# Performance work log

Hardware: AMD Instinct MI355X
Metric: run time of the kernel (lower is better)

## Reference

```python
import jax, jax.numpy as jnp
import numpy as np

N_AGENTS = 8
N_ACTIONS = 16
SAMPLE = 16
STATE_DIM = 256
EMBED = 256
IN_DIM = N_AGENTS * N_ACTIONS + STATE_DIM  # 384


def setup_inputs() -> dict:
    key = jax.random.key(0)
    ks = jax.random.split(key, 12)
    bs, t = 32, 32
    s = 0.05
    return {
        "states": jax.random.normal(ks[0], (bs, t, STATE_DIM), jnp.float32),
        "agent_qs": jax.random.normal(ks[1], (bs, t, N_AGENTS, N_ACTIONS), jnp.float32),
        "W1": jax.random.normal(ks[2], (IN_DIM, EMBED), jnp.float32) * s,
        "b1": jnp.zeros((EMBED,), jnp.float32),
        "W2": jax.random.normal(ks[3], (EMBED, EMBED), jnp.float32) * s,
        "b2": jnp.zeros((EMBED,), jnp.float32),
        "W3": jax.random.normal(ks[4], (EMBED, 1), jnp.float32) * s,
        "b3": jnp.zeros((1,), jnp.float32),
        "Vw1": jax.random.normal(ks[5], (STATE_DIM, EMBED), jnp.float32) * s,
        "Vb1": jnp.zeros((EMBED,), jnp.float32),
        "Vw2": jax.random.normal(ks[6], (EMBED, 1), jnp.float32) * s,
        "Vb2": jnp.zeros((1,), jnp.float32),
    }


def reference(states, agent_qs, W1, b1, W2, b2, W3, b3, Vw1, Vb1, Vw2, Vb2):
    bs, t = states.shape[0], states.shape[1]
    B = bs * t
    A, NA, S, sd = N_AGENTS, N_ACTIONS, SAMPLE, STATE_DIM
    st = states.reshape(B, sd)
    qs = agent_qs.reshape(B, A, NA)

    # --- sample grand coalitions (random permutation per (B,S) row) ---
    perm_key = jax.random.key(42)
    u = jax.random.uniform(perm_key, (B, S, A))
    pos = jnp.argsort(u, axis=-1)          # grand_coalitions_pos: agent i -> position pos[i]
    inv = jnp.argsort(pos, axis=-1)        # grand_coalitions: position j -> agent inv[j]

    indiv = jax.nn.one_hot(pos, A, dtype=st.dtype)                         # (B,S,A,A)
    subcoal = (jnp.arange(A)[None, None, None, :] <= pos[..., None]).astype(st.dtype)
    no_i = subcoal - indiv                                                 # coalition members excl. self

    # reorder agent qs along position dim: reordered[b,s,j,:] = qs[b, inv[b,s,j], :]
    reordered = jnp.take_along_axis(
        jnp.broadcast_to(qs[:, None], (B, S, A, NA)), inv[..., None], axis=2)

    # (B,S,A,A,NA): detach contribution of other coalition members
    coal = (jax.lax.stop_gradient(reordered[:, :, None] * no_i[..., None])
            + reordered[:, :, None] * indiv[..., None])

    x = coal.reshape(B * S * A, A * NA)
    stx = jnp.broadcast_to(st[:, None, None], (B, S, A, sd)).reshape(B * S * A, sd)
    inp = jnp.concatenate([stx, x], axis=1)

    h = jax.nn.relu(inp @ W1 + b1)
    h = jax.nn.relu(h @ W2 + b2)
    advs = h @ W3 + b3
    v = jax.nn.relu(stx @ Vw1 + Vb1) @ Vw2 + Vb2

    marginal = (advs + v).reshape(B, S, A)
    shapley = marginal.mean(axis=1)        # mean over samples
    return shapley.reshape(bs, t, A)
```

## Files before the change

kernel.cpp:

```cpp
#include <hip/hip_runtime.h>


#define A_N   8
#define NA_N  16
#define S_N   16
#define SD    256
#define EMB   256
#define B_TOT 1024

typedef __bf16 bf16x8 __attribute__((ext_vector_type(8)));
typedef float  f32x4  __attribute__((ext_vector_type(4)));

__device__ __forceinline__ f32x4 splat4(float v) {
  f32x4 x; x[0] = v; x[1] = v; x[2] = v; x[3] = v; return x;
}
__device__ __forceinline__ bf16x8 zero8() {
  bf16x8 z;
#pragma unroll
  for (int j = 0; j < 8; ++j) z[j] = (__bf16)0.0f;
  return z;
}

__device__ __forceinline__ float jax_uniform(unsigned idx) {
  const unsigned ks0 = 0u, ks1 = 42u, ks2 = 0x1BD11BDAu ^ 42u;
  unsigned x0 = 0u + ks0;
  unsigned x1 = idx + ks1;
#define TF_RND(r) { x0 += x1; x1 = (x1 << (r)) | (x1 >> (32 - (r))); x1 ^= x0; }
  TF_RND(13) TF_RND(15) TF_RND(26) TF_RND(6)  x0 += ks1; x1 += ks2 + 1u;
  TF_RND(17) TF_RND(29) TF_RND(16) TF_RND(24) x0 += ks2; x1 += ks0 + 2u;
  TF_RND(13) TF_RND(15) TF_RND(26) TF_RND(6)  x0 += ks0; x1 += ks1 + 3u;
  TF_RND(17) TF_RND(29) TF_RND(16) TF_RND(24) x0 += ks1; x1 += ks2 + 4u;
  TF_RND(13) TF_RND(15) TF_RND(26) TF_RND(6)  x0 += ks2; x1 += ks0 + 5u;
#undef TF_RND
  const unsigned bits = x0 ^ x1;
  return __uint_as_float((bits >> 9) | 0x3F800000u) - 1.0f;
}

__global__ __launch_bounds__(256) void prep_kernel(
    const float* __restrict__ states, const float* __restrict__ W1,
    const float* __restrict__ b1, const float* __restrict__ Vw1,
    const float* __restrict__ Vb1, const float* __restrict__ Vw2,
    const float* __restrict__ Vb2, float* __restrict__ sW,
    float* __restrict__ vout) {
  __shared__ float st_l[2][SD];
  __shared__ float red_l[2][4];
  const int b0 = blockIdx.x * 2;
  const int n = threadIdx.x;

#pragma unroll
  for (int i = 0; i < 2; ++i) st_l[i][n] = states[(b0 + i) * SD + n];
  __syncthreads();

  float aS[2], aV[2];
  const float b1n = b1[n], vb1n = Vb1[n];
#pragma unroll
  for (int i = 0; i < 2; ++i) { aS[i] = b1n; aV[i] = vb1n; }

#pragma unroll 8
  for (int k = 0; k < SD; ++k) {
    const float wv = W1[k * EMB + n];
    const float vw = Vw1[k * EMB + n];
#pragma unroll
    for (int i = 0; i < 2; ++i) {
      const float s = st_l[i][k];
      aS[i] = fmaf(s, wv, aS[i]);
      aV[i] = fmaf(s, vw, aV[i]);
    }
  }
#pragma unroll
  for (int i = 0; i < 2; ++i) sW[(b0 + i) * EMB + n] = aS[i];

  const float vw2 = Vw2[n];
#pragma unroll
  for (int i = 0; i < 2; ++i) {
    float c = fmaxf(aV[i], 0.f) * vw2;
#pragma unroll
    for (int off = 32; off; off >>= 1) c += __shfl_down(c, off);
    if ((n & 63) == 0) red_l[i][n >> 6] = c;
  }
  __syncthreads();
  if (n < 2)
    vout[b0 + n] = red_l[n][0] + red_l[n][1] + red_l[n][2] + red_l[n][3] + Vb2[0];
}

__global__ __launch_bounds__(256) void pack_kernel(
    const float* __restrict__ W1, const float* __restrict__ W2,
    __bf16* __restrict__ W1b_bf, __bf16* __restrict__ W2_bf) {
  const int ts = blockIdx.x * 256 + threadIdx.x;
  if (ts < 4096) {
    const int t = ts >> 10, rem = ts & 1023, u = rem >> 6, L = rem & 63;
    const int q = L >> 4, l15 = L & 15;
#pragma unroll
    for (int j = 0; j < 8; ++j) {
      const int k = t * 32 + q * 8 + j, nn = u * 16 + l15;
      W1b_bf[ts * 8 + j] = (__bf16)W1[(SD + k) * EMB + nn];
    }
  } else {
    const int ts2 = ts - 4096;
    const int t = ts2 >> 10, rem = ts2 & 1023, u = rem >> 6, L = rem & 63;
    const int q = L >> 4, l15 = L & 15;
#pragma unroll
    for (int j = 0; j < 8; ++j) {
      const int k = t * 32 + q * 8 + j, nn = u * 16 + l15;
      W2_bf[ts2 * 8 + j] = (__bf16)W2[k * EMB + nn];
    }
  }
}

__global__ __launch_bounds__(256, 4) void main_kernel(
    const float* __restrict__ agent_qs, const float* __restrict__ b2g,
    const float* __restrict__ W3, const float* __restrict__ b3,
    const float* __restrict__ sW, const float* __restrict__ vv,
    const __bf16* __restrict__ W1b_bf, const __bf16* __restrict__ W2_bf,
    float* __restrict__ out) {
  __shared__ bf16x8 h1_l[32 * 64];
  __shared__ __attribute__((aligned(16))) __bf16 qs_bf[A_N * NA_N];
  __shared__ float u_l[128];
  __shared__ int   inv_l[128];
  __shared__ int   pos_l[128];
  __shared__ float adv_part[4][64];
  __shared__ float marg_l[128];

  const int b = blockIdx.x;
  const int n = threadIdx.x;
  const int w = n >> 6, L = n & 63, q = L >> 4, l15 = L & 15;

  if (n < 128) {
    qs_bf[n] = (__bf16)agent_qs[b * 128 + n];
    u_l[n] = jax_uniform((unsigned)(b * 128 + n));
  }
  __syncthreads();

  if (n < 128) {
    const int s = n >> 3, a = n & 7;
    const float u = u_l[n];
    int r = 0;
#pragma unroll
    for (int a2 = 0; a2 < A_N; ++a2) {
      const float u2 = u_l[s * 8 + a2];
      r += (u2 < u || (u2 == u && a2 < a)) ? 1 : 0;
    }
    inv_l[n] = r;
    pos_l[s * 8 + r] = a;
  }
  __syncthreads();

  const int i_pref  = l15 & 7;
  const int sl_half = l15 >> 3;
  const int jq      = q >> 1;
  const int na0     = (q & 1) * 8;

  for (int p = 0; p < 2; ++p) {
#pragma unroll 1
    for (int nh = 0; nh < 2; ++nh) {
      f32x4 acc[4][2];
#pragma unroll
      for (int i = 0; i < 2; ++i) {
        const float sv = sW[b * EMB + (w * 4 + nh * 2 + i) * 16 + l15];
#pragma unroll
        for (int mt = 0; mt < 4; ++mt) acc[mt][i] = splat4(sv);
      }
#pragma unroll 2
      for (int t = 0; t < 4; ++t) {
        const int jcoal = t * 2 + jq;
        const bool on = (jcoal <= i_pref);
        bf16x8 bfr[2];
#pragma unroll
        for (int i = 0; i < 2; ++i)
          bfr[i] = *(const bf16x8*)
              &W1b_bf[((t * 16 + w * 4 + nh * 2 + i) * 64 + L) * 8];
#pragma unroll
        for (int mt = 0; mt < 4; ++mt) {
          const int ag = inv_l[(p * 8 + mt * 2 + sl_half) * 8 + jcoal];
          const bf16x8 qv = *(const bf16x8*)&qs_bf[ag * NA_N + na0];
          const bf16x8 af = on ? qv : zero8();
#pragma unroll
          for (int i = 0; i < 2; ++i)
            acc[mt][i] = __builtin_amdgcn_mfma_f32_16x16x32_bf16(
                af, bfr[i], acc[mt][i], 0, 0, 0);
        }
      }
      __bf16* h1e = (__bf16*)h1_l;
#pragma unroll
      for (int i = 0; i < 2; ++i) {
        const int c = (w * 4 + nh * 2 + i) * 16 + l15;
        const int t2 = c >> 5, q2 = (c >> 3) & 3, j2 = l15 & 7;
#pragma unroll
        for (int mt = 0; mt < 4; ++mt) {
#pragma unroll
          for (int r = 0; r < 4; ++r) {
            const float v = fmaxf(acc[mt][i][r], 0.f);
            h1e[(((t2 * 4 + mt) * 64) + q2 * 16 + q * 4 + r) * 8 + j2] =
                (__bf16)v;
          }
        }
      }
    }
    __syncthreads();

    float psum[4][4];
#pragma unroll
    for (int mt = 0; mt < 4; ++mt)
#pragma unroll
      for (int r = 0; r < 4; ++r) psum[mt][r] = 0.f;

#pragma unroll 1
    for (int nh = 0; nh < 2; ++nh) {
      f32x4 acc[4][2];
#pragma unroll
      for (int i = 0; i < 2; ++i) {
        const float bv = b2g[(w * 4 + nh * 2 + i) * 16 + l15];
#pragma unroll
        for (int mt = 0; mt < 4; ++mt) acc[mt][i] = splat4(bv);
      }
#pragma unroll 2
      for (int t = 0; t < 8; ++t) {
        bf16x8 bfr[2];
#pragma unroll
        for (int i = 0; i < 2; ++i)
          bfr[i] = *(const bf16x8*)
              &W2_bf[((t * 16 + w * 4 + nh * 2 + i) * 64 + L) * 8];
#pragma unroll
        for (int mt = 0; mt < 4; ++mt) {
          const bf16x8 af = h1_l[(t * 4 + mt) * 64 + L];
#pragma unroll
          for (int i = 0; i < 2; ++i)
            acc[mt][i] = __builtin_amdgcn_mfma_f32_16x16x32_bf16(
                af, bfr[i], acc[mt][i], 0, 0, 0);
        }
      }
#pragma unroll
      for (int i = 0; i < 2; ++i) {
        const float w3v = W3[(w * 4 + nh * 2 + i) * 16 + l15];
#pragma unroll
        for (int mt = 0; mt < 4; ++mt)
#pragma unroll
          for (int r = 0; r < 4; ++r)
            psum[mt][r] = fmaf(fmaxf(acc[mt][i][r], 0.f), w3v, psum[mt][r]);
      }
    }

#pragma unroll
    for (int mt = 0; mt < 4; ++mt) {
#pragma unroll
      for (int r = 0; r < 4; ++r) {
        float sum = psum[mt][r];
#pragma unroll
        for (int off = 1; off < 16; off <<= 1) sum += __shfl_xor(sum, off);
        if (l15 == 0) adv_part[w][mt * 16 + q * 4 + r] = sum;
      }
    }
    __syncthreads();
    if (n < 64)
      marg_l[p * 64 + n] = adv_part[0][n] + adv_part[1][n] +
                           adv_part[2][n] + adv_part[3][n];
    __syncthreads();
  }

  if (n < A_N) {
    float sh = 0.f;
#pragma unroll
    for (int s = 0; s < S_N; ++s) sh += marg_l[s * 8 + pos_l[s * 8 + n]];
    out[b * A_N + n] = sh * (1.f / 16.f) + b3[0] + vv[b];
  }
}

extern "C" void kernel_launch(void* const* d_in, const int* in_sizes, int n_in,
                              void* d_out, int out_size, void* d_ws,
                              size_t ws_size, hipStream_t stream) {
  const float* states   = (const float*)d_in[0];
  const float* agent_qs = (const float*)d_in[1];
  const float* W1       = (const float*)d_in[2];
  const float* b1       = (const float*)d_in[3];
  const float* W2       = (const float*)d_in[4];
  const float* b2       = (const float*)d_in[5];
  const float* W3       = (const float*)d_in[6];
  const float* b3       = (const float*)d_in[7];
  const float* Vw1      = (const float*)d_in[8];
  const float* Vb1      = (const float*)d_in[9];
  const float* Vw2      = (const float*)d_in[10];
  const float* Vb2      = (const float*)d_in[11];
  float* out = (float*)d_out;

  char* ws = (char*)d_ws;
  float*  sW     = (float*)(ws);
  float*  vv     = (float*)(ws + 1048576);
  __bf16* W1b_bf = (__bf16*)(ws + 1052672);
  __bf16* W2_bf  = (__bf16*)(ws + 1118208);

  prep_kernel<<<512, 256, 0, stream>>>(states, W1, b1, Vw1, Vb1, Vw2, Vb2,
                                       sW, vv);
  pack_kernel<<<48, 256, 0, stream>>>(W1, W2, W1b_bf, W2_bf);
  main_kernel<<<B_TOT, 256, 0, stream>>>(agent_qs, b2, W3, b3, sW, vv,
                                         W1b_bf, W2_bf, out);
}
```

Before: 123.0 us.

## Merge prep/pack kernels, skip zero coalition MFMAs, widen tiles, swizzle LDS

Folds the weight-packing kernel into the prep kernel to drop one launch. Reorders the main kernel's first-layer M tiles so each tile maps to one coalition position, which lets it skip the MFMAs whose inputs are entirely masked to zero. Both GEMM stages now handle four N columns per wave in one pass instead of two half passes, with biases and W3 preloaded into registers. The h1 shared-memory layout gets an XOR swizzle to avoid bank conflicts, and the final gather is remapped to match. Raising register use may cut occupancy, so launch bounds drop from 4 to 3 blocks.

```diff
diff --git a/kernel.cpp b/kernel.cpp
--- a/kernel.cpp
+++ b/kernel.cpp
@@ -36,14 +36,39 @@
   return __uint_as_float((bits >> 9) | 0x3F800000u) - 1.0f;
 }
 
-__global__ __launch_bounds__(256) void prep_kernel(
+__global__ __launch_bounds__(256) void prep_pack_kernel(
     const float* __restrict__ states, const float* __restrict__ W1,
     const float* __restrict__ b1, const float* __restrict__ Vw1,
     const float* __restrict__ Vb1, const float* __restrict__ Vw2,
-    const float* __restrict__ Vb2, float* __restrict__ sW,
-    float* __restrict__ vout) {
+    const float* __restrict__ Vb2, const float* __restrict__ W2,
+    float* __restrict__ sW, float* __restrict__ vout,
+    __bf16* __restrict__ W1b_bf, __bf16* __restrict__ W2_bf) {
   __shared__ float st_l[2][SD];
   __shared__ float red_l[2][4];
+
+  if (blockIdx.x >= 512) {
+    const int ts = (blockIdx.x - 512) * 256 + threadIdx.x;
+    if (ts < 4096) {
+      const int t = ts >> 10, rem = ts & 1023, u = rem >> 6, Lp = rem & 63;
+      const int qp = Lp >> 4, l15p = Lp & 15;
+#pragma unroll
+      for (int j = 0; j < 8; ++j) {
+        const int k = t * 32 + qp * 8 + j, nn = u * 16 + l15p;
+        W1b_bf[ts * 8 + j] = (__bf16)W1[(SD + k) * EMB + nn];
+      }
+    } else {
+      const int ts2 = ts - 4096;
+      const int t = ts2 >> 10, rem = ts2 & 1023, u = rem >> 6, Lp = rem & 63;
+      const int qp = Lp >> 4, l15p = Lp & 15;
+#pragma unroll
+      for (int j = 0; j < 8; ++j) {
+        const int k = t * 32 + qp * 8 + j, nn = u * 16 + l15p;
+        W2_bf[ts2 * 8 + j] = (__bf16)W2[k * EMB + nn];
+      }
+    }
+    return;
+  }
+
   const int b0 = blockIdx.x * 2;
   const int n = threadIdx.x;
 
@@ -83,31 +108,7 @@
     vout[b0 + n] = red_l[n][0] + red_l[n][1] + red_l[n][2] + red_l[n][3] + Vb2[0];
 }
 
-__global__ __launch_bounds__(256) void pack_kernel(
-    const float* __restrict__ W1, const float* __restrict__ W2,
-    __bf16* __restrict__ W1b_bf, __bf16* __restrict__ W2_bf) {
-  const int ts = blockIdx.x * 256 + threadIdx.x;
-  if (ts < 4096) {
-    const int t = ts >> 10, rem = ts & 1023, u = rem >> 6, L = rem & 63;
-    const int q = L >> 4, l15 = L & 15;
-#pragma unroll
-    for (int j = 0; j < 8; ++j) {
-      const int k = t * 32 + q * 8 + j, nn = u * 16 + l15;
-      W1b_bf[ts * 8 + j] = (__bf16)W1[(SD + k) * EMB + nn];
-    }
-  } else {
-    const int ts2 = ts - 4096;
-    const int t = ts2 >> 10, rem = ts2 & 1023, u = rem >> 6, L = rem & 63;
-    const int q = L >> 4, l15 = L & 15;
-#pragma unroll
-    for (int j = 0; j < 8; ++j) {
-      const int k = t * 32 + q * 8 + j, nn = u * 16 + l15;
-      W2_bf[ts2 * 8 + j] = (__bf16)W2[k * EMB + nn];
-    }
-  }
-}
-
-__global__ __launch_bounds__(256, 4) void main_kernel(
+__global__ __launch_bounds__(256, 3) void main_kernel(
     const float* __restrict__ agent_qs, const float* __restrict__ b2g,
     const float* __restrict__ W3, const float* __restrict__ b3,
     const float* __restrict__ sW, const float* __restrict__ vv,
@@ -124,6 +125,11 @@
   const int b = blockIdx.x;
   const int n = threadIdx.x;
   const int w = n >> 6, L = n & 63, q = L >> 4, l15 = L & 15;
+  const int s7 = l15 & 7;
+  const int sl = l15 >> 3;
+  const int jq = q >> 1;
+  const int na0 = (q & 1) * 8;
+  const int Lsw = L ^ ((L >> 3) & 3);
 
   if (n < 128) {
     qs_bf[n] = (__bf16)agent_qs[b * 128 + n];
@@ -145,100 +151,99 @@
   }
   __syncthreads();
 
-  const int i_pref  = l15 & 7;
-  const int sl_half = l15 >> 3;
-  const int jq      = q >> 1;
-  const int na0     = (q & 1) * 8;
-
+  const bool diag_on = (jq <= sl);
+
+  float svv[4], bvv[4], w3v[4];
+#pragma unroll
+  for (int c = 0; c < 4; ++c) {
+    const int col = (w * 4 + c) * 16 + l15;
+    svv[c] = sW[b * EMB + col];
+    bvv[c] = b2g[col];
+    w3v[c] = W3[col];
+  }
+
+#pragma unroll 1
   for (int p = 0; p < 2; ++p) {
-#pragma unroll 1
-    for (int nh = 0; nh < 2; ++nh) {
-      f32x4 acc[4][2];
-#pragma unroll
-      for (int i = 0; i < 2; ++i) {
-        const float sv = sW[b * EMB + (w * 4 + nh * 2 + i) * 16 + l15];
-#pragma unroll
-        for (int mt = 0; mt < 4; ++mt) acc[mt][i] = splat4(sv);
-      }
-#pragma unroll 2
-      for (int t = 0; t < 4; ++t) {
-        const int jcoal = t * 2 + jq;
-        const bool on = (jcoal <= i_pref);
-        bf16x8 bfr[2];
-#pragma unroll
-        for (int i = 0; i < 2; ++i)
-          bfr[i] = *(const bf16x8*)
-              &W1b_bf[((t * 16 + w * 4 + nh * 2 + i) * 64 + L) * 8];
+    f32x4 acc[4][4];
+#pragma unroll
+    for (int c = 0; c < 4; ++c)
+#pragma unroll
+      for (int mt = 0; mt < 4; ++mt) acc[mt][c] = splat4(svv[c]);
+
+    const int invbase = (p * 8 + s7) * 8;
+#pragma unroll
+    for (int t = 0; t < 4; ++t) {
+      const int ag = inv_l[invbase + 2 * t + jq];
+      const bf16x8 afb = *(const bf16x8*)&qs_bf[ag * NA_N + na0];
+      const bf16x8 afd = diag_on ? afb : zero8();
+#pragma unroll
+      for (int c = 0; c < 4; ++c) {
+        const bf16x8 bfr = *(const bf16x8*)
+            &W1b_bf[((t * 16 + w * 4 + c) * 64 + L) * 8];
 #pragma unroll
         for (int mt = 0; mt < 4; ++mt) {
-          const int ag = inv_l[(p * 8 + mt * 2 + sl_half) * 8 + jcoal];
-          const bf16x8 qv = *(const bf16x8*)&qs_bf[ag * NA_N + na0];
-          const bf16x8 af = on ? qv : zero8();
-#pragma unroll
-          for (int i = 0; i < 2; ++i)
-            acc[mt][i] = __builtin_amdgcn_mfma_f32_16x16x32_bf16(
-                af, bfr[i], acc[mt][i], 0, 0, 0);
+          if (mt < t) continue;
+          acc[mt][c] = __builtin_amdgcn_mfma_f32_16x16x32_bf16(
+              (mt == t) ? afd : afb, bfr, acc[mt][c], 0, 0, 0);
         }
       }
+    }
+
+    {
       __bf16* h1e = (__bf16*)h1_l;
 #pragma unroll
-      for (int i = 0; i < 2; ++i) {
-        const int c = (w * 4 + nh * 2 + i) * 16 + l15;
-        const int t2 = c >> 5, q2 = (c >> 3) & 3, j2 = l15 & 7;
+      for (int c = 0; c < 4; ++c) {
+        const int X = w * 4 + c;
+        const int hi = (X & 1) * 2 + sl;
+        const int xr = (q >> 1) | ((hi & 1) << 1);
 #pragma unroll
         for (int mt = 0; mt < 4; ++mt) {
+          const int ub = ((X >> 1) * 4 + mt) * 64 + (hi << 4);
 #pragma unroll
           for (int r = 0; r < 4; ++r) {
-            const float v = fmaxf(acc[mt][i][r], 0.f);
-            h1e[(((t2 * 4 + mt) * 64) + q2 * 16 + q * 4 + r) * 8 + j2] =
-                (__bf16)v;
+            const float v = fmaxf(acc[mt][c][r], 0.f);
+            const int u = ub + ((q * 4 + r) ^ xr);
+            h1e[u * 8 + s7] = (__bf16)v;
           }
         }
       }
     }
     __syncthreads();
 
+    f32x4 acc2[4][4];
+#pragma unroll
+    for (int c = 0; c < 4; ++c)
+#pragma unroll
+      for (int mt = 0; mt < 4; ++mt) acc2[mt][c] = splat4(bvv[c]);
+
+#pragma unroll
+    for (int t = 0; t < 8; ++t) {
+      bf16x8 af[4];
+#pragma unroll
+      for (int mt = 0; mt < 4; ++mt) af[mt] = h1_l[(t * 4 + mt) * 64 + Lsw];
+#pragma unroll
+      for (int c = 0; c < 4; ++c) {
+        const bf16x8 bfr = *(const bf16x8*)
+            &W2_bf[((t * 16 + w * 4 + c) * 64 + L) * 8];
+#pragma unroll
+        for (int mt = 0; mt < 4; ++mt)
+          acc2[mt][c] = __builtin_amdgcn_mfma_f32_16x16x32_bf16(
+              af[mt], bfr, acc2[mt][c], 0, 0, 0);
+      }
+    }
+
     float psum[4][4];
 #pragma unroll
     for (int mt = 0; mt < 4; ++mt)
 #pragma unroll
       for (int r = 0; r < 4; ++r) psum[mt][r] = 0.f;
-
-#pragma unroll 1
-    for (int nh = 0; nh < 2; ++nh) {
-      f32x4 acc[4][2];
-#pragma unroll
-      for (int i = 0; i < 2; ++i) {
-        const float bv = b2g[(w * 4 + nh * 2 + i) * 16 + l15];
-#pragma unroll
-        for (int mt = 0; mt < 4; ++mt) acc[mt][i] = splat4(bv);
-      }
-#pragma unroll 2
-      for (int t = 0; t < 8; ++t) {
-        bf16x8 bfr[2];
-#pragma unroll
-        for (int i = 0; i < 2; ++i)
-          bfr[i] = *(const bf16x8*)
-              &W2_bf[((t * 16 + w * 4 + nh * 2 + i) * 64 + L) * 8];
-#pragma unroll
-        for (int mt = 0; mt < 4; ++mt) {
-          const bf16x8 af = h1_l[(t * 4 + mt) * 64 + L];
-#pragma unroll
-          for (int i = 0; i < 2; ++i)
-            acc[mt][i] = __builtin_amdgcn_mfma_f32_16x16x32_bf16(
-                af, bfr[i], acc[mt][i], 0, 0, 0);
-        }
-      }
-#pragma unroll
-      for (int i = 0; i < 2; ++i) {
-        const float w3v = W3[(w * 4 + nh * 2 + i) * 16 + l15];
-#pragma unroll
-        for (int mt = 0; mt < 4; ++mt)
-#pragma unroll
-          for (int r = 0; r < 4; ++r)
-            psum[mt][r] = fmaf(fmaxf(acc[mt][i][r], 0.f), w3v, psum[mt][r]);
-      }
-    }
+#pragma unroll
+    for (int c = 0; c < 4; ++c)
+#pragma unroll
+      for (int mt = 0; mt < 4; ++mt)
+#pragma unroll
+        for (int r = 0; r < 4; ++r)
+          psum[mt][r] = fmaf(fmaxf(acc2[mt][c][r], 0.f), w3v[c], psum[mt][r]);
 
 #pragma unroll
     for (int mt = 0; mt < 4; ++mt) {
@@ -260,7 +265,10 @@
   if (n < A_N) {
     float sh = 0.f;
 #pragma unroll
-    for (int s = 0; s < S_N; ++s) sh += marg_l[s * 8 + pos_l[s * 8 + n]];
+    for (int s = 0; s < S_N; ++s) {
+      const int pr = pos_l[s * 8 + n];
+      sh += marg_l[((s >> 3) << 6) + pr * 8 + (s & 7)];
+    }
     out[b * A_N + n] = sh * (1.f / 16.f) + b3[0] + vv[b];
   }
 }
@@ -288,9 +296,8 @@
   __bf16* W1b_bf = (__bf16*)(ws + 1052672);
   __bf16* W2_bf  = (__bf16*)(ws + 1118208);
 
-  prep_kernel<<<512, 256, 0, stream>>>(states, W1, b1, Vw1, Vb1, Vw2, Vb2,
-                                       sW, vv);
-  pack_kernel<<<48, 256, 0, stream>>>(W1, W2, W1b_bf, W2_bf);
+  prep_pack_kernel<<<560, 256, 0, stream>>>(states, W1, b1, Vw1, Vb1, Vw2,
+                                            Vb2, W2, sW, vv, W1b_bf, W2_bf);
   main_kernel<<<B_TOT, 256, 0, stream>>>(agent_qs, b2, W3, b3, sW, vv,
                                          W1b_bf, W2_bf, out);
 }
```

Result: slower. 285.0 us (+131.7%).
